# Optimization experiments

Hardware: AMD Instinct MI355X
Metric: run time of the kernel (lower is better)

## Reference

```python
import jax, jax.numpy as jnp
import numpy as np

B = 2
L = 512                         # latent dim
NF = [64, 128, 256, 512, 512]   # _get_num_features(2*base_features=64, 64, max=512)


def _rn(key, shape, scale=1.0):
    return scale * jax.random.normal(key, shape, dtype=jnp.float32)


def _blur_up(x):
    """upfirdn2d: 2x upsample + FIR blur with resample_kernel [1,3,3,1], gain=factor**2."""
    k = jnp.array([1.0, 3.0, 3.0, 1.0], dtype=x.dtype)
    kk = jnp.outer(k, k)
    kk = kk / kk.sum() * 4.0  # gain = 2**2
    c = x.shape[-1]
    kern = jnp.broadcast_to(kk[:, :, None, None], (4, 4, 1, c))
    return jax.lax.conv_general_dilated(
        x, kern, (1, 1), ((2, 2), (2, 2)), lhs_dilation=(2, 2),
        dimension_numbers=('NHWC', 'HWIO', 'NHWC'), feature_group_count=c)


def _mod_conv(x, latent, w, b, sw, sb, demodulate):
    """StyleGAN2 modulated conv. x:(B,H,W,Cin), w:(kh,kw,Cin,Cout), style affine (L,Cin)."""
    s = latent @ sw + sb                             # (B,Cin) style
    ww = w[None] * s[:, None, None, :, None]         # (B,kh,kw,Cin,Cout)
    if demodulate:
        d = jax.lax.rsqrt(jnp.sum(ww * ww, axis=(1, 2, 3)) + 1e-8)  # (B,Cout)
        ww = ww * d[:, None, None, None, :]
    def per_sample(xi, wi):
        return jax.lax.conv_general_dilated(
            xi[None], wi, (1, 1), 'SAME',
            dimension_numbers=('NHWC', 'HWIO', 'NHWC'))[0]
    return jax.vmap(per_sample)(x, ww) + b


def _forward(latents, const, w0, b0, sw0, sb0, ns0, noise0, wr0, br0, swr0, sbr0,
             wu1, bu1, swu1, sbu1, wc1, bc1, swc1, sbc1, wr1, br1, swr1, sbr1,
             wu2, bu2, swu2, sbu2, wc2, bc2, swc2, sbc2, wr2, br2, swr2, sbr2,
             wu3, bu3, swu3, sbu3, wc3, bc3, swc3, sbc3, wr3, br3, swr3, sbr3,
             wu4, bu4, swu4, sbu4, wc4, bc4, swc4, sbc4, wr4, br4, swr4, sbr4):
    act = lambda t: jax.nn.leaky_relu(t, 0.01)
    b = latents.shape[0]
    lat = latents.reshape(b, 2, 5, latents.shape[-1])  # (B,2,n_levels,L)
    # first layer at 4x4: modulated conv + noise + leaky_relu (only layer with noise, per source)
    y = _mod_conv(jnp.tile(const[None], (b, 1, 1, 1)), lat[:, 0, 0], w0, b0, sw0, sb0, True)
    y = act(y + ns0 * noise0)
    rgb = act(_mod_conv(y, lat[:, 0, 1], wr0, br0, swr0, sbr0, False))
    ups = [(wu1, bu1, swu1, sbu1), (wu2, bu2, swu2, sbu2), (wu3, bu3, swu3, sbu3), (wu4, bu4, swu4, sbu4)]
    cvs = [(wc1, bc1, swc1, sbc1), (wc2, bc2, swc2, sbc2), (wc3, bc3, swc3, sbc3), (wc4, bc4, swc4, sbc4)]
    rgbs = [(wr1, br1, swr1, sbr1), (wr2, br2, swr2, sbr2), (wr3, br3, swr3, sbr3), (wr4, br4, swr4, sbr4)]
    for i in range(1, 5):
        wu, bu, swu, sbu = ups[i - 1]
        wc, bc, swc, sbc = cvs[i - 1]
        wr, br, swr, sbr = rgbs[i - 1]
        y = _mod_conv(_blur_up(y), lat[:, i - 1, 1], wu, bu, swu, sbu, True)
        # plain ModulatedConv2D 3x3 (no noise/activation in the source loop)
        y = _mod_conv(y, lat[:, i, 0], wc, bc, swc, sbc, True)
        # to_rgb (no demod) + skip accumulation of FIR-upsampled previous rgb
        rgb = act(_mod_conv(y, lat[:, i, 1], wr, br, swr, sbr, False)) + _blur_up(rgb)
    return rgb  # (B,64,64,3)


reference = _forward


def setup_inputs():
    key = jax.random.key(0)
    ks = iter(jax.random.split(key, 80))
    inp = {}
    inp['latents'] = _rn(next(ks), (B, 2 * 5, L))
    inp['const'] = _rn(next(ks), (4, 4, NF[-1]))
    def mod(pfx, kh, cin, cout):
        inp['w' + pfx] = _rn(next(ks), (kh, kh, cin, cout), (kh * kh * cin) ** -0.5)
        inp['b' + pfx] = jnp.zeros((cout,), jnp.float32)
        inp['sw' + pfx] = _rn(next(ks), (L, cin), L ** -0.5)
        inp['sb' + pfx] = jnp.ones((cin,), jnp.float32)
    mod('0', 3, NF[-1], NF[-1])
    inp['ns0'] = 0.1 * _rn(next(ks), (1, 1, 1, 1))
    inp['noise0'] = _rn(next(ks), (B, 4, 4, 1))
    mod('r0', 1, NF[-1], 3)
    cprev = NF[-1]
    for i in range(1, 5):
        c = NF[i]
        mod('u%d' % i, 3, cprev, c)
        mod('c%d' % i, 3, c, c)
        mod('r%d' % i, 1, c, 3)
        cprev = c
    return inp
```

## Files before the change

### kernel.cpp

```cpp
#include <hip/hip_runtime.h>

#define LEAKY(v) ((v) > 0.f ? (v) : 0.01f * (v))

typedef __attribute__((ext_vector_type(8))) short bf16x8;
typedef __attribute__((ext_vector_type(4))) short bf16x4;
typedef __attribute__((ext_vector_type(4))) float floatx4;

__device__ inline unsigned short f2bf(float f) {
  unsigned u = __float_as_uint(f);
  unsigned r = u + 0x7FFFu + ((u >> 16) & 1u);
  return (unsigned short)(r >> 16);
}

__device__ inline bf16x8 ld_frag8(const unsigned short* p) {
  bf16x4 lo = *(const bf16x4*)p;
  bf16x4 hi = *(const bf16x4*)(p + 4);
  return __builtin_shufflevector(lo, hi, 0, 1, 2, 3, 4, 5, 6, 7);
}

struct StyleDesc { const float* sw; const float* sb; int row; int cin; };
struct StyleArgs { StyleDesc d[14]; };
struct W2D { const float* w; int cinLog; int coutLog; int start; int w2off; };
struct W2Args { W2D d[9]; int total4; };
struct WPD { const float* src; unsigned short* dst; int cin; int cout; int start; };
struct WPArgs { WPD d[6]; int total; };

__device__ void style_body(int bid, const float* __restrict__ lat, const StyleArgs& A,
                           float* __restrict__ S)
{
  int chunk = bid & 1, b = (bid >> 1) & 1, sid = bid >> 2;
  StyleDesc d = A.d[sid];
  int ci = chunk * 256 + threadIdx.x;
  if (ci >= d.cin) return;
  const float* l = lat + (size_t)b * (10 * 512) + d.row * 512;
  float a0 = 0.f, a1 = 0.f, a2 = 0.f, a3 = 0.f, a4 = 0.f, a5 = 0.f, a6 = 0.f, a7 = 0.f;
  const float* wp = d.sw + ci;
  size_t st = d.cin;
  for (int k = 0; k < 512; k += 8) {
    a0 += l[k] * wp[0];
    a1 += l[k + 1] * wp[st];
    a2 += l[k + 2] * wp[2 * st];
    a3 += l[k + 3] * wp[3 * st];
    a4 += l[k + 4] * wp[4 * st];
    a5 += l[k + 5] * wp[5 * st];
    a6 += l[k + 6] * wp[6 * st];
    a7 += l[k + 7] * wp[7 * st];
    wp += 8 * st;
  }
  S[sid * 1024 + b * 512 + ci] = d.sb[ci] + ((a0 + a1) + (a2 + a3)) + ((a4 + a5) + (a6 + a7));
}

__device__ void w2_body(int idx, const W2Args& A, float* __restrict__ W2)
{
  if (idx >= A.total4) return;
  int c = 0;
  while (c < 8 && idx >= A.d[c + 1].start) c++;
  W2D d = A.d[c];
  int rel = idx - d.start;
  int co4Log = d.coutLog - 2;
  int ci = rel >> co4Log;
  int co = (rel & ((1 << co4Log) - 1)) << 2;
  size_t ktStride = (size_t)(1 << d.cinLog) << d.coutLog;
  const float* p = d.w + ((size_t)ci << d.coutLog) + co;
  float4 acc = {0.f, 0.f, 0.f, 0.f};
#pragma unroll
  for (int kt = 0; kt < 9; kt++) {
    float4 v = *(const float4*)(p + kt * ktStride);
    acc.x += v.x * v.x; acc.y += v.y * v.y; acc.z += v.z * v.z; acc.w += v.w * v.w;
  }
  *(float4*)(W2 + d.w2off + ((size_t)ci << d.coutLog) + co) = acc;
}

__device__ void wprep_body(int chunk, const WPArgs& A)
{
  if (chunk >= A.total) return;
  int c = 0;
  while (c < 5 && chunk >= A.d[c + 1].start) c++;
  WPD d = A.d[c];
  int rel = chunk - d.start;
  int cpc = d.cin * 9 / 8;
  int co = rel / cpc;
  int k0 = (rel - co * cpc) * 8;
  int cig = k0 / 288;
  int r = k0 - cig * 288;
  int kt = r >> 5;
  int cibase = cig * 32 + (r & 31);
  const float* sp = d.src + (size_t)(kt * d.cin + cibase) * d.cout + co;
  size_t st = d.cout;
  unsigned r0 = f2bf(sp[0]) | ((unsigned)f2bf(sp[st]) << 16);
  unsigned r1 = f2bf(sp[2 * st]) | ((unsigned)f2bf(sp[3 * st]) << 16);
  unsigned r2 = f2bf(sp[4 * st]) | ((unsigned)f2bf(sp[5 * st]) << 16);
  unsigned r3 = f2bf(sp[6 * st]) | ((unsigned)f2bf(sp[7 * st]) << 16);
  uint4 v = {r0, r1, r2, r3};
  *(uint4*)(d.dst + (size_t)co * (d.cin * 9) + k0) = v;
}

__global__ __launch_bounds__(256) void prep_all_kernel(
    const float* __restrict__ lat, StyleArgs SA, W2Args WA, WPArgs PA,
    float* __restrict__ S, float* __restrict__ W2, int styleBlocks, int w2Blocks)
{
  int bid = blockIdx.x;
  if (bid < styleBlocks) { style_body(bid, lat, SA, S); return; }
  bid -= styleBlocks;
  if (bid < w2Blocks) { w2_body(bid * 256 + threadIdx.x, WA, W2); return; }
  bid -= w2Blocks;
  wprep_body(bid * 256 + threadIdx.x, PA);
}

struct D2D { int w2off; int sid; int did; int cin; int cout; int start; };
struct D2Args { D2D d[9]; };

__global__ __launch_bounds__(256) void demod2_all_kernel(
    D2Args A, const float* __restrict__ W2, const float* __restrict__ S,
    float* __restrict__ Dout)
{
  __shared__ float red[256];
  int bid = blockIdx.x;
  int c = 0;
  while (c < 8 && bid >= A.d[c + 1].start) c++;
  D2D d = A.d[c];
  int rel = bid - d.start;
  int chunksPerB = d.cout >> 6;
  int b = rel / chunksPerB;
  int coc = rel - b * chunksPerB;
  int co = coc * 64 + (threadIdx.x & 63);
  int slice = threadIdx.x >> 6;
  const float* sv = S + d.sid * 1024 + b * 512;
  const float* wp = W2 + d.w2off + co;
  float a0 = 0.f, a1 = 0.f, a2 = 0.f, a3 = 0.f, a4 = 0.f, a5 = 0.f, a6 = 0.f, a7 = 0.f;
  for (int r = slice; r < d.cin; r += 32) {
    float s0 = sv[r];          a0 += s0 * s0 * wp[(size_t)r * d.cout];
    float s1 = sv[r + 4];      a1 += s1 * s1 * wp[(size_t)(r + 4) * d.cout];
    float s2 = sv[r + 8];      a2 += s2 * s2 * wp[(size_t)(r + 8) * d.cout];
    float s3 = sv[r + 12];     a3 += s3 * s3 * wp[(size_t)(r + 12) * d.cout];
    float s4 = sv[r + 16];     a4 += s4 * s4 * wp[(size_t)(r + 16) * d.cout];
    float s5 = sv[r + 20];     a5 += s5 * s5 * wp[(size_t)(r + 20) * d.cout];
    float s6 = sv[r + 24];     a6 += s6 * s6 * wp[(size_t)(r + 24) * d.cout];
    float s7 = sv[r + 28];     a7 += s7 * s7 * wp[(size_t)(r + 28) * d.cout];
  }
  red[threadIdx.x] = ((a0 + a1) + (a2 + a3)) + ((a4 + a5) + (a6 + a7));
  __syncthreads();
  if (threadIdx.x < 64) {
    float a = red[threadIdx.x] + red[threadIdx.x + 64] + red[threadIdx.x + 128] + red[threadIdx.x + 192];
    Dout[d.did * 1024 + b * 512 + co] = rsqrtf(a + 1e-8f);
  }
}

__device__ inline void blur_taps(int o, int* r0, int* r1, float* w0, float* w1)
{
  if ((o & 1) == 0) { *r0 = (o >> 1) - 1; *w0 = 1.f; *r1 = (o >> 1); *w1 = 3.f; }
  else              { *r0 = (o - 1) >> 1; *w0 = 3.f; *r1 = ((o - 1) >> 1) + 1; *w1 = 1.f; }
}

__global__ __launch_bounds__(256) void prep_up_kernel(
    const float* __restrict__ y, int Hc, int C,
    const float* __restrict__ s, unsigned short* __restrict__ out)
{
  int b = blockIdx.y;
  int W2 = Hc * 2;
  int pix = blockIdx.x;
  int oy = pix / W2, ox = pix - oy * W2;
  int ry0, ry1, rx0, rx1; float wy0, wy1, wx0, wx1;
  blur_taps(oy, &ry0, &ry1, &wy0, &wy1);
  blur_taps(ox, &rx0, &rx1, &wx0, &wx1);
  bool vy0 = (ry0 >= 0 && ry0 < Hc), vy1 = (ry1 >= 0 && ry1 < Hc);
  bool vx0 = (rx0 >= 0 && rx0 < Hc), vx1 = (rx1 >= 0 && rx1 < Hc);
  const float* base = y + (size_t)b * Hc * Hc * C;
  unsigned short* ob = out + (((size_t)b * W2 + oy) * W2 + ox) * C;
  const float* sv = s + b * 512;
  for (int c = threadIdx.x; c < C; c += 256) {
    float acc = 0.f;
    if (vy0) {
      const float* r = base + (size_t)(ry0 * Hc) * C;
      if (vx0) acc += wy0 * wx0 * r[(size_t)rx0 * C + c];
      if (vx1) acc += wy0 * wx1 * r[(size_t)rx1 * C + c];
    }
    if (vy1) {
      const float* r = base + (size_t)(ry1 * Hc) * C;
      if (vx0) acc += wy1 * wx0 * r[(size_t)rx0 * C + c];
      if (vx1) acc += wy1 * wx1 * r[(size_t)rx1 * C + c];
    }
    ob[c] = f2bf(acc * (1.f / 16.f) * sv[c]);
  }
}

__global__ __launch_bounds__(256) void mfma_conv_kernel(
    const unsigned short* __restrict__ xp, int H, int WLOG, int Cin, int Cout,
    const unsigned short* __restrict__ wT,
    const float* __restrict__ bias, const float* __restrict__ dmod,
    float* __restrict__ outF, unsigned short* __restrict__ outBf,
    const float* __restrict__ sNext)
{
  extern __shared__ unsigned short sm[];
  const int W = 1 << WLOG;
  const int Rt = 128 >> WLOG;
  const int PR = Rt + 2, PC = W + 2;
  const int patchU = PR * PC * 36;
  unsigned short* Bw = sm + patchU;

  const int tid = threadIdx.x;
  const int wave = tid >> 6;
  const int lane = tid & 63;
  const int q = lane >> 4;
  const int l15 = lane & 15;

  const int HW = H << WLOG;
  const int m0 = blockIdx.x << 7;
  const int b = m0 / HW;
  const int y0 = (m0 - b * HW) >> WLOG;
  const int co0 = blockIdx.y << 6;
  const int Kp = Cin * 9;
  const unsigned short* xb = xp + (size_t)b * HW * Cin;

  const int pSlots = PR * PC * 4;
  int pLds[5], pSrc[5];
#pragma unroll
  for (int i = 0; i < 5; i++) {
    int sidx = tid + i * 256;
    pLds[i] = -1; pSrc[i] = -1;
    if (sidx < pSlots) {
      int pidx = sidx >> 2, part = sidx & 3;
      int pr = pidx / PC, pc = pidx - pr * PC;
      int gy = y0 + pr - 1, gx = pc - 1;
      pLds[i] = pidx * 36 + part * 8;
      if ((unsigned)gy < (unsigned)H && (unsigned)gx < (unsigned)W)
        pSrc[i] = ((gy << WLOG) + gx) * Cin + part * 8;
    }
  }
  int bLds[9], bSrc[9];
#pragma unroll
  for (int i = 0; i < 9; i++) {
    int sidx = tid + i * 256;
    int n = sidx / 36, c16 = sidx - n * 36;
    bLds[i] = n * 292 + c16 * 8;
    bSrc[i] = (co0 + n) * Kp + c16 * 8;
  }

  floatx4 zero = {0.f, 0.f, 0.f, 0.f};
  floatx4 acc[2][4];
#pragma unroll
  for (int mi = 0; mi < 2; mi++)
#pragma unroll
    for (int s = 0; s < 4; s++) acc[mi][s] = zero;

  const int mA0 = wave * 32 + l15;
  const int mA1 = mA0 + 16;
  const int aBase0 = ((mA0 >> WLOG) * PC + (mA0 & (W - 1))) * 36 + q * 8;
  const int aBase1 = ((mA1 >> WLOG) * PC + (mA1 & (W - 1))) * 36 + q * 8;
  const int bBase = l15 * 292 + q * 8;

  const int nGroups = Cin >> 5;
  for (int g = 0; g < nGroups; g++) {
    __syncthreads();
    {
      const int gci = g << 5;
#pragma unroll
      for (int i = 0; i < 5; i++) {
        if (pLds[i] >= 0) {
          uint4 v = {0u, 0u, 0u, 0u};
          if (pSrc[i] >= 0) v = *(const uint4*)(xb + pSrc[i] + gci);
          uint2 lo = {v.x, v.y}, hi = {v.z, v.w};
          *(uint2*)(sm + pLds[i]) = lo;
          *(uint2*)(sm + pLds[i] + 4) = hi;
        }
      }
      const int gw = g * 288;
#pragma unroll
      for (int i = 0; i < 9; i++) {
        uint4 v = *(const uint4*)(wT + bSrc[i] + gw);
        uint2 lo = {v.x, v.y}, hi = {v.z, v.w};
        *(uint2*)(Bw + bLds[i]) = lo;
        *(uint2*)(Bw + bLds[i] + 4) = hi;
      }
    }
    __syncthreads();
#pragma unroll
    for (int kt = 0; kt < 9; kt++) {
      const int ky = kt / 3, kx = kt - (kt / 3) * 3;
      const int ao = (ky * PC + kx) * 36;
      bf16x8 a0 = ld_frag8(sm + aBase0 + ao);
      bf16x8 a1 = ld_frag8(sm + aBase1 + ao);
      const int bo = bBase + kt * 32;
#pragma unroll
      for (int s = 0; s < 4; s++) {
        bf16x8 bb = ld_frag8(Bw + bo + s * (16 * 292));
        acc[0][s] = __builtin_amdgcn_mfma_f32_16x16x32_bf16(a0, bb, acc[0][s], 0, 0, 0);
        acc[1][s] = __builtin_amdgcn_mfma_f32_16x16x32_bf16(a1, bb, acc[1][s], 0, 0, 0);
      }
    }
  }

#pragma unroll
  for (int s = 0; s < 4; s++) {
    const int co = co0 + s * 16 + l15;
    const float dm = dmod[b * 512 + co];
    const float bv = bias[co];
    const float sn = sNext ? sNext[b * 512 + co] : 0.f;
#pragma unroll
    for (int mi = 0; mi < 2; mi++) {
#pragma unroll
      for (int r = 0; r < 4; r++) {
        const int mloc = wave * 32 + mi * 16 + q * 4 + r;
        const int py = y0 + (mloc >> WLOG);
        const int px = mloc & (W - 1);
        const size_t oidx = (((size_t)b * H + py) * W + px) * Cout + co;
        const float v = acc[mi][s][r] * dm + bv;
        if (outF) outF[oidx] = v;
        if (outBf) outBf[oidx] = f2bf(v * sn);
      }
    }
  }
}

template<int PIX, int NCI4>
__global__ __launch_bounds__(256) void modconv_splitk_kernel(
    const float* __restrict__ x, size_t xBStride, int H, int W, int cinShift,
    int Cout,
    const float* __restrict__ w, const float* __restrict__ s,
    float* __restrict__ partial)
{
  constexpr int NCI = NCI4 * 4;
  constexpr int CLOG = (NCI == 16) ? 4 : (NCI == 32) ? 5 : 6;
  extern __shared__ float lds[];
  const int COLS = PIX + 2;
  const int tid = threadIdx.x;
  const int nthr = blockDim.x;
  const int b = blockIdx.y;
  const int z = blockIdx.z;
  const int ci0 = z << CLOG;
  const int wb = W / PIX;
  const int row = blockIdx.x / wb;
  const int x0 = (blockIdx.x % wb) * PIX;

  const float* xb = x + (size_t)b * xBStride;
  const float* sv = s + b * 512;

  const int tot = 3 * COLS << CLOG;
  for (int idx = tid; idx < tot; idx += nthr) {
    int cil = idx & (NCI - 1);
    int t = idx >> CLOG;
    int col = t % COLS;
    int ry = t / COLS;
    int gy = row + ry - 1;
    int gx = x0 + col - 1;
    float v = 0.f;
    if (gy >= 0 && gy < H && gx >= 0 && gx < W)
      v = xb[((size_t)(gy * W + gx) << cinShift) + ci0 + cil] * sv[ci0 + cil];
    lds[idx] = v;
  }
  __syncthreads();

  float acc0[PIX];
  float acc1[PIX];
#pragma unroll
  for (int p = 0; p < PIX; p++) { acc0[p] = 0.f; acc1[p] = 0.f; }
  const int co0 = tid;
  const int co1 = tid + nthr;
  const bool a0 = co0 < Cout;
  const bool a1 = co1 < Cout;
  const int d01 = nthr;

  const float4* ldsv = (const float4*)lds;
  constexpr int cin4Shift = CLOG - 2;

  for (int kt = 0; kt < 9; kt++) {
    int ky = kt / 3, kx = kt % 3;
    const float* wr = w + ((size_t)(kt << cinShift) + ci0) * Cout + co0;
#pragma unroll
    for (int c4 = 0; c4 < NCI4; c4++) {
      float wA0 = 0.f, wA1 = 0.f, wA2 = 0.f, wA3 = 0.f;
      float wB0 = 0.f, wB1 = 0.f, wB2 = 0.f, wB3 = 0.f;
      const float* wq = wr + (size_t)c4 * 4 * Cout;
      if (a0) { wA0 = wq[0]; }
      if (a1) { wB0 = wq[d01]; }
      if (a0) { wA1 = wq[Cout]; }
      if (a1) { wB1 = wq[Cout + d01]; }
      if (a0) { wA2 = wq[2 * Cout]; }
      if (a1) { wB2 = wq[2 * Cout + d01]; }
      if (a0) { wA3 = wq[3 * Cout]; }
      if (a1) { wB3 = wq[3 * Cout + d01]; }
#pragma unroll
      for (int p = 0; p < PIX; p++) {
        float4 v = ldsv[((ky * COLS + kx + p) << cin4Shift) + c4];
        acc0[p] += v.x * wA0; acc0[p] += v.y * wA1; acc0[p] += v.z * wA2; acc0[p] += v.w * wA3;
        acc1[p] += v.x * wB0; acc1[p] += v.y * wB1; acc1[p] += v.z * wB2; acc1[p] += v.w * wB3;
      }
    }
  }

  const int HW = H * W;
  float* pb = partial + ((size_t)(z * gridDim.y + b) * HW + row * W + x0) * Cout;
#pragma unroll
  for (int p = 0; p < PIX; p++) {
    if (a0) pb[(size_t)p * Cout + co0] = acc0[p];
    if (a1) pb[(size_t)p * Cout + co1] = acc1[p];
  }
}

__global__ __launch_bounds__(128) void modconv_splitk_blur_kernel(
    const float* __restrict__ y, const float* __restrict__ w,
    const float* __restrict__ s, float* __restrict__ partial)
{
  extern __shared__ float lds[];
  const int tid = threadIdx.x;
  const int b = blockIdx.y;
  const int z = blockIdx.z;
  const int ci0 = z << 4;
  const int row = blockIdx.x;

  const float* yb = y + (size_t)b * 16 * 512;
  const float* sv = s + b * 512;

  for (int idx = tid; idx < 480; idx += 128) {
    int cil = idx & 15;
    int t = idx >> 4;
    int col = t % 10;
    int ry = t / 10;
    int gy = row + ry - 1;
    int gx = col - 1;
    float v = 0.f;
    if ((unsigned)gy < 8u && (unsigned)gx < 8u) {
      int ry0, ry1, rx0, rx1; float wy0, wy1, wx0, wx1;
      blur_taps(gy, &ry0, &ry1, &wy0, &wy1);
      blur_taps(gx, &rx0, &rx1, &wx0, &wx1);
      bool vy0 = (ry0 >= 0 && ry0 < 4), vy1 = (ry1 >= 0 && ry1 < 4);
      bool vx0 = (rx0 >= 0 && rx0 < 4), vx1 = (rx1 >= 0 && rx1 < 4);
      int ci = ci0 + cil;
      float acc = 0.f;
      if (vy0 && vx0) acc += wy0 * wx0 * yb[((ry0 * 4 + rx0) << 9) + ci];
      if (vy0 && vx1) acc += wy0 * wx1 * yb[((ry0 * 4 + rx1) << 9) + ci];
      if (vy1 && vx0) acc += wy1 * wx0 * yb[((ry1 * 4 + rx0) << 9) + ci];
      if (vy1 && vx1) acc += wy1 * wx1 * yb[((ry1 * 4 + rx1) << 9) + ci];
      v = acc * (1.f / 16.f) * sv[ci];
    }
    lds[idx] = v;
  }
  __syncthreads();

  float acc0[8];
#pragma unroll
  for (int p = 0; p < 8; p++) acc0[p] = 0.f;
  const int co0 = tid;
  const float4* ldsv = (const float4*)lds;

  for (int kt = 0; kt < 9; kt++) {
    int ky = kt / 3, kx = kt % 3;
    const float* wr = w + ((size_t)(kt << 9) + ci0) * 128 + co0;
#pragma unroll
    for (int c4 = 0; c4 < 4; c4++) {
      const float* wq = wr + (size_t)c4 * 4 * 128;
      float wA0 = wq[0];
      float wA1 = wq[128];
      float wA2 = wq[256];
      float wA3 = wq[384];
#pragma unroll
      for (int p = 0; p < 8; p++) {
        float4 v = ldsv[((ky * 10 + kx + p) << 2) + c4];
        acc0[p] += v.x * wA0; acc0[p] += v.y * wA1; acc0[p] += v.z * wA2; acc0[p] += v.w * wA3;
      }
    }
  }

  float* pb = partial + ((size_t)(z * gridDim.y + b) * 64 + row * 8) * 128;
#pragma unroll
  for (int p = 0; p < 8; p++) pb[(size_t)p * 128 + co0] = acc0[p];
}

__global__ __launch_bounds__(256) void splitk_epi_kernel(
    const float* __restrict__ partial, int nz, int M, int Cout, int HW,
    const float* __restrict__ dmod, const float* __restrict__ bias,
    float* __restrict__ out)
{
  int idx = blockIdx.x * 256 + threadIdx.x;
  if (idx >= M * Cout) return;
  int m = idx / Cout;
  int co = idx - m * Cout;
  int b = m / HW;
  float acc = 0.f;
  for (int z = 0; z < nz; z++) acc += partial[(size_t)z * M * Cout + idx];
  out[idx] = acc * dmod[b * 512 + co] + bias[co];
}

__global__ void epirgb_kernel(
    const float* __restrict__ P, int nz, int HW, int Cout, int W,
    const float* __restrict__ dmod, const float* __restrict__ bias,
    const float* __restrict__ noise, const float* __restrict__ ns, int doAct,
    const float* __restrict__ sR, const float* __restrict__ wR, const float* __restrict__ bR,
    const float* __restrict__ prev,
    float* __restrict__ yout, float* __restrict__ rgbout)
{
  __shared__ float red[24];
  int b = blockIdx.x / HW;
  int pix = blockIdx.x - b * HW;
  int co = threadIdx.x;
  int m = b * HW + pix;
  float acc = 0.f;
  for (int z = 0; z < nz; z++) acc += P[((size_t)(z * 2 + b) * HW + pix) * Cout + co];
  float v = acc * dmod[b * 512 + co] + bias[co];
  if (noise) v += ns[0] * noise[m];
  if (doAct) v = LEAKY(v);
  yout[(size_t)m * Cout + co] = v;
  float t = v * sR[b * 512 + co];
  float r0 = t * wR[co * 3 + 0];
  float r1 = t * wR[co * 3 + 1];
  float r2 = t * wR[co * 3 + 2];
  for (int off = 32; off > 0; off >>= 1) {
    r0 += __shfl_down(r0, off);
    r1 += __shfl_down(r1, off);
    r2 += __shfl_down(r2, off);
  }
  int wv = threadIdx.x >> 6, lane = threadIdx.x & 63;
  if (lane == 0) { red[wv * 3 + 0] = r0; red[wv * 3 + 1] = r1; red[wv * 3 + 2] = r2; }
  __syncthreads();
  if (threadIdx.x == 0) {
    int nw = blockDim.x >> 6;
    float s0 = bR[0], s1 = bR[1], s2 = bR[2];
    for (int w = 0; w < nw; w++) { s0 += red[w * 3]; s1 += red[w * 3 + 1]; s2 += red[w * 3 + 2]; }
    s0 = LEAKY(s0); s1 = LEAKY(s1); s2 = LEAKY(s2);
    if (prev) {
      int oy = pix / W, ox = pix - (pix / W) * W;
      int Hp = W >> 1;
      int ry0, ry1, rx0, rx1; float wy0, wy1, wx0, wx1;
      blur_taps(oy, &ry0, &ry1, &wy0, &wy1);
      blur_taps(ox, &rx0, &rx1, &wx0, &wx1);
      bool vy0 = (ry0 >= 0 && ry0 < Hp), vy1 = (ry1 >= 0 && ry1 < Hp);
      bool vx0 = (rx0 >= 0 && rx0 < Hp), vx1 = (rx1 >= 0 && rx1 < Hp);
      const float* base = prev + (size_t)b * Hp * Hp * 3;
      float a0 = 0.f, a1 = 0.f, a2 = 0.f;
      if (vy0 && vx0) { const float* qq = base + (size_t)(ry0 * Hp + rx0) * 3; float wg = wy0 * wx0; a0 += wg * qq[0]; a1 += wg * qq[1]; a2 += wg * qq[2]; }
      if (vy0 && vx1) { const float* qq = base + (size_t)(ry0 * Hp + rx1) * 3; float wg = wy0 * wx1; a0 += wg * qq[0]; a1 += wg * qq[1]; a2 += wg * qq[2]; }
      if (vy1 && vx0) { const float* qq = base + (size_t)(ry1 * Hp + rx0) * 3; float wg = wy1 * wx0; a0 += wg * qq[0]; a1 += wg * qq[1]; a2 += wg * qq[2]; }
      if (vy1 && vx1) { const float* qq = base + (size_t)(ry1 * Hp + rx1) * 3; float wg = wy1 * wx1; a0 += wg * qq[0]; a1 += wg * qq[1]; a2 += wg * qq[2]; }
      s0 += a0 * (1.f / 16.f); s1 += a1 * (1.f / 16.f); s2 += a2 * (1.f / 16.f);
    }
    rgbout[(size_t)m * 3 + 0] = s0;
    rgbout[(size_t)m * 3 + 1] = s1;
    rgbout[(size_t)m * 3 + 2] = s2;
  }
}

__global__ __launch_bounds__(64) void rgb_kernel(
    const float* __restrict__ y, int H, int W, int Cin,
    const float* __restrict__ w, const float* __restrict__ bias,
    const float* __restrict__ s, const float* __restrict__ prev,
    float* __restrict__ out)
{
  int b = blockIdx.y;
  int pix = blockIdx.x;
  int oy = pix / W, ox = pix % W;
  const float* xp = y + (((size_t)b * H + oy) * W + ox) * Cin;
  const float* sv = s + b * 512;
  float p0 = 0.f, p1 = 0.f, p2 = 0.f;
  for (int ci = threadIdx.x; ci < Cin; ci += 64) {
    float v = xp[ci] * sv[ci];
    p0 += v * w[ci * 3 + 0];
    p1 += v * w[ci * 3 + 1];
    p2 += v * w[ci * 3 + 2];
  }
  for (int off = 32; off > 0; off >>= 1) {
    p0 += __shfl_down(p0, off);
    p1 += __shfl_down(p1, off);
    p2 += __shfl_down(p2, off);
  }
  if (threadIdx.x == 0) {
    float r0 = p0 + bias[0], r1 = p1 + bias[1], r2 = p2 + bias[2];
    float sk0 = 0.f, sk1 = 0.f, sk2 = 0.f;
    if (prev) {
      int Hp = H >> 1, Wp = W >> 1;
      int ry0, ry1, rx0, rx1; float wy0, wy1, wx0, wx1;
      blur_taps(oy, &ry0, &ry1, &wy0, &wy1);
      blur_taps(ox, &rx0, &rx1, &wx0, &wx1);
      bool vy0 = (ry0 >= 0 && ry0 < Hp), vy1 = (ry1 >= 0 && ry1 < Hp);
      bool vx0 = (rx0 >= 0 && rx0 < Wp), vx1 = (rx1 >= 0 && rx1 < Wp);
      const float* base = prev + (size_t)b * Hp * Wp * 3;
      float a0 = 0.f, a1 = 0.f, a2 = 0.f;
      if (vy0 && vx0) { const float* qq = base + (size_t)(ry0 * Wp + rx0) * 3; float wg = wy0 * wx0; a0 += wg * qq[0]; a1 += wg * qq[1]; a2 += wg * qq[2]; }
      if (vy0 && vx1) { const float* qq = base + (size_t)(ry0 * Wp + rx1) * 3; float wg = wy0 * wx1; a0 += wg * qq[0]; a1 += wg * qq[1]; a2 += wg * qq[2]; }
      if (vy1 && vx0) { const float* qq = base + (size_t)(ry1 * Wp + rx0) * 3; float wg = wy1 * wx0; a0 += wg * qq[0]; a1 += wg * qq[1]; a2 += wg * qq[2]; }
      if (vy1 && vx1) { const float* qq = base + (size_t)(ry1 * Wp + rx1) * 3; float wg = wy1 * wx1; a0 += wg * qq[0]; a1 += wg * qq[1]; a2 += wg * qq[2]; }
      sk0 = a0 * (1.f / 16.f); sk1 = a1 * (1.f / 16.f); sk2 = a2 * (1.f / 16.f);
    }
    float* ob = out + (((size_t)b * H + oy) * W + ox) * 3;
    ob[0] = LEAKY(r0) + sk0;
    ob[1] = LEAKY(r1) + sk1;
    ob[2] = LEAKY(r2) + sk2;
  }
}

extern "C" void kernel_launch(void* const* d_in, const int* in_sizes, int n_in,
                              void* d_out, int out_size, void* d_ws, size_t ws_size,
                              hipStream_t stream)
{
  auto F = [&](int k) { return (const float*)d_in[k]; };
  const float* latents = F(0);
  const float* cnst = F(1);
  const float* w0 = F(2);  const float* b0 = F(3);  const float* sw0 = F(4);  const float* sb0 = F(5);
  const float* ns0 = F(6); const float* noise0 = F(7);
  const float* wr0 = F(8); const float* br0 = F(9); const float* swr0 = F(10); const float* sbr0 = F(11);
  const float *wu[4], *bu[4], *swu[4], *sbu[4];
  const float *wc[4], *bc[4], *swc[4], *sbc[4];
  const float *wr[4], *br_[4], *swr[4], *sbr[4];
  int k = 12;
  for (int l = 0; l < 4; l++) {
    wu[l] = F(k++); bu[l] = F(k++); swu[l] = F(k++); sbu[l] = F(k++);
    wc[l] = F(k++); bc[l] = F(k++); swc[l] = F(k++); sbc[l] = F(k++);
    wr[l] = F(k++); br_[l] = F(k++); swr[l] = F(k++); sbr[l] = F(k++);
  }

  float* ws = (float*)d_ws;
  float* S = ws;
  float* D = S + 14 * 1024;
  float* W2 = D + 9 * 1024;
  float* bufA = W2 + 1359872;
  float* bufB = bufA + 2 * 64 * 64 * 512;
  float* rgbA = bufB + 2 * 64 * 64 * 512;
  float* rgbB = rgbA + 2 * 64 * 64 * 3;
  float* P = rgbB + 2 * 64 * 64 * 3;
  unsigned short* u16 = (unsigned short*)(P + 524288);
  unsigned short* xprepA = u16;
  unsigned short* xprepB = xprepA + 2 * 64 * 64 * 512;
  unsigned short* wT[6];
  {
    unsigned short* p = xprepB + 2 * 64 * 64 * 512;
    int wsz[6] = {9 * 128 * 256, 9 * 256 * 256, 9 * 256 * 512, 9 * 512 * 512, 9 * 512 * 512, 9 * 512 * 512};
    for (int i = 0; i < 6; i++) { wT[i] = p; p += wsz[i]; }
  }

  const int B = 2;
  const int NFa[5] = {64, 128, 256, 512, 512};
  int cprev0[4] = {512, 128, 256, 512};
  int rowu[4] = {1, 6, 6, 6};

  const float* cw[9]  = {w0, wu[0], wc[0], wu[1], wc[1], wu[2], wc[2], wu[3], wc[3]};
  int cinL[9]  = {9, 9, 7, 7, 8, 8, 9, 9, 9};
  int coutL[9] = {9, 7, 7, 8, 8, 9, 9, 9, 9};
  int sidOf[9] = {0, 2, 3, 5, 6, 8, 9, 11, 12};
  int didOf[9] = {0, 1, 2, 3, 4, 5, 6, 7, 8};

  int w2off[9];
  {
    StyleArgs SA;
    SA.d[0] = {sw0, sb0, 0, 512};
    SA.d[1] = {swr0, sbr0, 1, 512};
    for (int l = 0; l < 4; l++) {
      int c = NFa[l + 1];
      SA.d[2 + l * 3] = {swu[l], sbu[l], rowu[l], cprev0[l]};
      SA.d[3 + l * 3] = {swc[l], sbc[l], 5, c};
      SA.d[4 + l * 3] = {swr[l], sbr[l], 6, c};
    }
    W2Args WA2;
    int w2start = 0, off = 0;
    for (int i = 0; i < 9; i++) {
      w2off[i] = off;
      WA2.d[i] = {cw[i], cinL[i], coutL[i], w2start, off};
      int elems = 1 << (cinL[i] + coutL[i]);
      w2start += elems >> 2;
      off += elems;
    }
    WA2.total4 = w2start;
    WPArgs WPA;
    {
      const float* srcs[6] = {wu[1], wc[1], wu[2], wc[2], wu[3], wc[3]};
      int cins[6] = {128, 256, 256, 512, 512, 512};
      int couts[6] = {256, 256, 512, 512, 512, 512};
      int start = 0;
      for (int i = 0; i < 6; i++) {
        WPA.d[i] = {srcs[i], wT[i], cins[i], couts[i], start};
        start += couts[i] * cins[i] * 9 / 8;
      }
      WPA.total = start;
    }
    int styleBlocks = 56;
    int w2Blocks = (WA2.total4 + 255) / 256;
    int wpBlocks = (WPA.total + 255) / 256;
    prep_all_kernel<<<dim3(styleBlocks + w2Blocks + wpBlocks), 256, 0, stream>>>(
        latents, SA, WA2, WPA, S, W2, styleBlocks, w2Blocks);
  }

  {
    D2Args DA;
    int start = 0;
    for (int i = 0; i < 9; i++) {
      int cout = 1 << coutL[i];
      DA.d[i] = {w2off[i], sidOf[i], didOf[i], 1 << cinL[i], cout, start};
      start += B * (cout >> 6);
    }
    demod2_all_kernel<<<dim3(start), 256, 0, stream>>>(DA, W2, S, D);
  }

  modconv_splitk_kernel<4, 4><<<dim3(4, B, 32), 256, (size_t)3 * 6 * 16 * 4, stream>>>(
      cnst, 0, 4, 4, 9, 512, w0, S, P);
  epirgb_kernel<<<dim3(B * 16), 512, 0, stream>>>(
      P, 32, 16, 512, 4, D, b0, noise0, ns0, 1,
      S + 1024, wr0, br0, nullptr, bufA, rgbA);

  modconv_splitk_blur_kernel<<<dim3(8, B, 32), 128, (size_t)480 * 4, stream>>>(
      bufA, wu[0], S + 2 * 1024, P);
  splitk_epi_kernel<<<dim3((128 * 128 + 255) / 256), 256, 0, stream>>>(
      P, 32, 128, 128, 64, D + 1 * 1024, bu[0], bufA);
  modconv_splitk_kernel<8, 4><<<dim3(8, B, 8), 128, (size_t)3 * 10 * 16 * 4, stream>>>(
      bufA, (size_t)64 * 128, 8, 8, 7, 128, wc[0], S + 3 * 1024, P);
  epirgb_kernel<<<dim3(B * 64), 128, 0, stream>>>(
      P, 8, 64, 128, 8, D + 2 * 1024, bc[0], nullptr, nullptr, 0,
      S + 4 * 1024, wr[0], br_[0], rgbA, bufB, rgbB);

  float* ybuf[4] = {bufB, bufA, bufB, bufA};
  float* rgbp = rgbB;
  const float* ysrc = bufB;
  int Hc = 8;
  for (int l = 1; l < 4; l++) {
    int c = NFa[l + 1];
    int cp = cprev0[l];
    int H2 = Hc * 2;
    int WLOG = (H2 == 16) ? 4 : (H2 == 32) ? 5 : 6;
    int wi = (l - 1) * 2;
    prep_up_kernel<<<dim3(H2 * H2, B), 256, 0, stream>>>(
        ysrc, Hc, cp, S + (2 + l * 3) * 1024, xprepA);
    {
      int PRu = (128 >> WLOG) + 2, PCu = H2 + 2;
      size_t lds = (size_t)(PRu * PCu * 36 + 64 * 292) * 2;
      mfma_conv_kernel<<<dim3((B * H2 * H2) / 128, c >> 6), 256, lds, stream>>>(
          xprepA, H2, WLOG, cp, c, wT[wi], bu[l], D + (1 + l * 2) * 1024,
          nullptr, xprepB, S + (3 + l * 3) * 1024);
    }
    float* yo = ybuf[l];
    {
      int PRu = (128 >> WLOG) + 2, PCu = H2 + 2;
      size_t lds = (size_t)(PRu * PCu * 36 + 64 * 292) * 2;
      mfma_conv_kernel<<<dim3((B * H2 * H2) / 128, c >> 6), 256, lds, stream>>>(
          xprepB, H2, WLOG, c, c, wT[wi + 1], bc[l], D + (2 + l * 2) * 1024,
          yo, nullptr, nullptr);
    }
    float* rout = (l == 3) ? (float*)d_out : ((rgbp == rgbA) ? rgbB : rgbA);
    rgb_kernel<<<dim3(H2 * H2, B), 64, 0, stream>>>(
        yo, H2, H2, c, wr[l], br_[l], S + (4 + l * 3) * 1024, rgbp, rout);
    rgbp = (rout == rgbA) ? rgbA : rgbB;
    ysrc = yo;
    Hc = H2;
  }
  (void)in_sizes; (void)n_in; (void)out_size; (void)ws_size;
}
```

Before: 629.9 us.

## Tile weight bf16 transpose through LDS and prefetch next K-group in MFMA conv

The weight prep step, which converts fp32 weights to the transposed bf16 layout, now works on 64x288 tiles staged in shared memory. Each block reads coalesced float4 rows and writes contiguous output rows, replacing the earlier strided scalar gathers per thread. The MFMA conv kernel also holds the next channel group's input and weight fragments in registers, loading them while the current group's MFMAs run, which hides global load latency. The costs are a 37KB static LDS buffer on every block of the prep kernel, which can lower occupancy for the style and w2 blocks, and more register pressure in the conv kernel.

```diff
diff --git a/kernel.cpp b/kernel.cpp
--- a/kernel.cpp
+++ b/kernel.cpp
@@ -22,8 +22,8 @@
 struct StyleArgs { StyleDesc d[14]; };
 struct W2D { const float* w; int cinLog; int coutLog; int start; int w2off; };
 struct W2Args { W2D d[9]; int total4; };
-struct WPD { const float* src; unsigned short* dst; int cin; int cout; int start; };
-struct WPArgs { WPD d[6]; int total; };
+struct WTD { const float* src; unsigned short* dst; int cinLog; int coutLog; int start; };
+struct WTArgs { WTD d[6]; int totalTiles; };
 
 __device__ void style_body(int bid, const float* __restrict__ lat, const StyleArgs& A,
                            float* __restrict__ S)
@@ -71,40 +71,52 @@
   *(float4*)(W2 + d.w2off + ((size_t)ci << d.coutLog) + co) = acc;
 }
 
-__device__ void wprep_body(int chunk, const WPArgs& A)
-{
-  if (chunk >= A.total) return;
+__device__ void wprep_tile_body(int tile, const WTArgs& A, unsigned short* __restrict__ tl)
+{
   int c = 0;
-  while (c < 5 && chunk >= A.d[c + 1].start) c++;
-  WPD d = A.d[c];
-  int rel = chunk - d.start;
-  int cpc = d.cin * 9 / 8;
-  int co = rel / cpc;
-  int k0 = (rel - co * cpc) * 8;
-  int cig = k0 / 288;
-  int r = k0 - cig * 288;
-  int kt = r >> 5;
-  int cibase = cig * 32 + (r & 31);
-  const float* sp = d.src + (size_t)(kt * d.cin + cibase) * d.cout + co;
-  size_t st = d.cout;
-  unsigned r0 = f2bf(sp[0]) | ((unsigned)f2bf(sp[st]) << 16);
-  unsigned r1 = f2bf(sp[2 * st]) | ((unsigned)f2bf(sp[3 * st]) << 16);
-  unsigned r2 = f2bf(sp[4 * st]) | ((unsigned)f2bf(sp[5 * st]) << 16);
-  unsigned r3 = f2bf(sp[6 * st]) | ((unsigned)f2bf(sp[7 * st]) << 16);
-  uint4 v = {r0, r1, r2, r3};
-  *(uint4*)(d.dst + (size_t)co * (d.cin * 9) + k0) = v;
+  while (c < 5 && tile >= A.d[c + 1].start) c++;
+  WTD d = A.d[c];
+  int rel = tile - d.start;
+  int coTiles = 1 << (d.coutLog - 6);
+  int cig = rel / coTiles;
+  int co0 = (rel - cig * coTiles) << 6;
+  int cin = 1 << d.cinLog, cout = 1 << d.coutLog;
+  int tid = threadIdx.x;
+  for (int slot = tid; slot < 288 * 16; slot += 256) {
+    int r = slot >> 4;
+    int co4 = slot & 15;
+    int kt = r >> 5, cisub = r & 31;
+    const float* sp = d.src + ((size_t)(kt * cin + (cig << 5) + cisub) << d.coutLog) + co0 + co4 * 4;
+    float4 v = *(const float4*)sp;
+    int cb = co4 * 4;
+    tl[(cb + 0) * 296 + r] = f2bf(v.x);
+    tl[(cb + 1) * 296 + r] = f2bf(v.y);
+    tl[(cb + 2) * 296 + r] = f2bf(v.z);
+    tl[(cb + 3) * 296 + r] = f2bf(v.w);
+  }
+  __syncthreads();
+  int Kp = cin * 9;
+  for (int slot = tid; slot < 64 * 36; slot += 256) {
+    int co = slot / 36, c8 = slot - (slot / 36) * 36;
+    bf16x4 lo = *(const bf16x4*)(tl + co * 296 + c8 * 8);
+    bf16x4 hi = *(const bf16x4*)(tl + co * 296 + c8 * 8 + 4);
+    unsigned short* op = d.dst + (size_t)(co0 + co) * Kp + cig * 288 + c8 * 8;
+    *(bf16x4*)op = lo;
+    *(bf16x4*)(op + 4) = hi;
+  }
 }
 
 __global__ __launch_bounds__(256) void prep_all_kernel(
-    const float* __restrict__ lat, StyleArgs SA, W2Args WA, WPArgs PA,
+    const float* __restrict__ lat, StyleArgs SA, W2Args WA, WTArgs TA,
     float* __restrict__ S, float* __restrict__ W2, int styleBlocks, int w2Blocks)
 {
+  __shared__ unsigned short tl[64 * 296];
   int bid = blockIdx.x;
   if (bid < styleBlocks) { style_body(bid, lat, SA, S); return; }
   bid -= styleBlocks;
   if (bid < w2Blocks) { w2_body(bid * 256 + threadIdx.x, WA, W2); return; }
   bid -= w2Blocks;
-  wprep_body(bid * 256 + threadIdx.x, PA);
+  if (bid < TA.totalTiles) wprep_tile_body(bid, TA, tl);
 }
 
 struct D2D { int w2off; int sid; int did; int cin; int cout; int start; };
@@ -250,30 +262,48 @@
   const int bBase = l15 * 292 + q * 8;
 
   const int nGroups = Cin >> 5;
+
+  uint4 pv[5], bv[9];
+  {
+#pragma unroll
+    for (int i = 0; i < 5; i++) {
+      uint4 v = {0u, 0u, 0u, 0u};
+      if (pLds[i] >= 0 && pSrc[i] >= 0) v = *(const uint4*)(xb + pSrc[i]);
+      pv[i] = v;
+    }
+#pragma unroll
+    for (int i = 0; i < 9; i++) bv[i] = *(const uint4*)(wT + bSrc[i]);
+  }
+
   for (int g = 0; g < nGroups; g++) {
     __syncthreads();
-    {
-      const int gci = g << 5;
+#pragma unroll
+    for (int i = 0; i < 5; i++) {
+      if (pLds[i] >= 0) {
+        uint2 lo = {pv[i].x, pv[i].y}, hi = {pv[i].z, pv[i].w};
+        *(uint2*)(sm + pLds[i]) = lo;
+        *(uint2*)(sm + pLds[i] + 4) = hi;
+      }
+    }
+#pragma unroll
+    for (int i = 0; i < 9; i++) {
+      uint2 lo = {bv[i].x, bv[i].y}, hi = {bv[i].z, bv[i].w};
+      *(uint2*)(Bw + bLds[i]) = lo;
+      *(uint2*)(Bw + bLds[i] + 4) = hi;
+    }
+    __syncthreads();
+    if (g + 1 < nGroups) {
+      const int gci = (g + 1) << 5;
+      const int gw = (g + 1) * 288;
 #pragma unroll
       for (int i = 0; i < 5; i++) {
-        if (pLds[i] >= 0) {
-          uint4 v = {0u, 0u, 0u, 0u};
-          if (pSrc[i] >= 0) v = *(const uint4*)(xb + pSrc[i] + gci);
-          uint2 lo = {v.x, v.y}, hi = {v.z, v.w};
-          *(uint2*)(sm + pLds[i]) = lo;
-          *(uint2*)(sm + pLds[i] + 4) = hi;
-        }
+        uint4 v = {0u, 0u, 0u, 0u};
+        if (pLds[i] >= 0 && pSrc[i] >= 0) v = *(const uint4*)(xb + pSrc[i] + gci);
+        pv[i] = v;
       }
-      const int gw = g * 288;
-#pragma unroll
-      for (int i = 0; i < 9; i++) {
-        uint4 v = *(const uint4*)(wT + bSrc[i] + gw);
-        uint2 lo = {v.x, v.y}, hi = {v.z, v.w};
-        *(uint2*)(Bw + bLds[i]) = lo;
-        *(uint2*)(Bw + bLds[i] + 4) = hi;
-      }
-    }
-    __syncthreads();
+#pragma unroll
+      for (int i = 0; i < 9; i++) bv[i] = *(const uint4*)(wT + bSrc[i] + gw);
+    }
 #pragma unroll
     for (int kt = 0; kt < 9; kt++) {
       const int ky = kt / 3, kx = kt - (kt / 3) * 3;
@@ -294,7 +324,7 @@
   for (int s = 0; s < 4; s++) {
     const int co = co0 + s * 16 + l15;
     const float dm = dmod[b * 512 + co];
-    const float bv = bias[co];
+    const float bv2 = bias[co];
     const float sn = sNext ? sNext[b * 512 + co] : 0.f;
 #pragma unroll
     for (int mi = 0; mi < 2; mi++) {
@@ -304,7 +334,7 @@
         const int py = y0 + (mloc >> WLOG);
         const int px = mloc & (W - 1);
         const size_t oidx = (((size_t)b * H + py) * W + px) * Cout + co;
-        const float v = acc[mi][s][r] * dm + bv;
+        const float v = acc[mi][s][r] * dm + bv2;
         if (outF) outF[oidx] = v;
         if (outBf) outBf[oidx] = f2bf(v * sn);
       }
@@ -658,23 +688,22 @@
       off += elems;
     }
     WA2.total4 = w2start;
-    WPArgs WPA;
+    WTArgs TA;
     {
       const float* srcs[6] = {wu[1], wc[1], wu[2], wc[2], wu[3], wc[3]};
-      int cins[6] = {128, 256, 256, 512, 512, 512};
-      int couts[6] = {256, 256, 512, 512, 512, 512};
+      int cinLg[6] = {7, 8, 8, 9, 9, 9};
+      int coutLg[6] = {8, 8, 9, 9, 9, 9};
       int start = 0;
       for (int i = 0; i < 6; i++) {
-        WPA.d[i] = {srcs[i], wT[i], cins[i], couts[i], start};
-        start += couts[i] * cins[i] * 9 / 8;
+        TA.d[i] = {srcs[i], wT[i], cinLg[i], coutLg[i], start};
+        start += (1 << (cinLg[i] - 5)) * (1 << (coutLg[i] - 6));
       }
-      WPA.total = start;
+      TA.totalTiles = start;
     }
     int styleBlocks = 56;
     int w2Blocks = (WA2.total4 + 255) / 256;
-    int wpBlocks = (WPA.total + 255) / 256;
-    prep_all_kernel<<<dim3(styleBlocks + w2Blocks + wpBlocks), 256, 0, stream>>>(
-        latents, SA, WA2, WPA, S, W2, styleBlocks, w2Blocks);
+    prep_all_kernel<<<dim3(styleBlocks + w2Blocks + TA.totalTiles), 256, 0, stream>>>(
+        latents, SA, WA2, TA, S, W2, styleBlocks, w2Blocks);
   }
 
   {
```

Result: faster. 553.5 us (-12.1%).
